# Kernel optimization log

Hardware: AMD Instinct MI355X
Metric: run time of the kernel (lower is better)

The kernel has to match this reference:

```python
import jax, jax.numpy as jnp
import numpy as np

B, S, INQ = 2048, 200, 120
POS_E = 8
H, QLEN, VLEN = 8, 16, 64
HID = H * VLEN  # 512
IN_F = INQ + POS_E  # 128
LN_EPS = 1e-5


def _css(x, W, b, Wc, bc):
    # CssModel: gated linear h1 * sigmoid(h1c)
    h1 = x @ W + b
    h1c = jax.nn.sigmoid(x @ Wc + bc)
    return h1 * h1c


def _layernorm(x, g, b):
    mu = jnp.mean(x, axis=-1, keepdims=True)
    var = jnp.var(x, axis=-1, keepdims=True)
    return (x - mu) * jax.lax.rsqrt(var + LN_EPS) * g + b


def setup_inputs() -> dict:
    key = jax.random.key(0)
    ks = jax.random.split(key, 16)
    d = {}
    d["posid"] = jax.random.randint(ks[0], (B, S), 0, 100, dtype=jnp.int64) if jax.config.jax_enable_x64 else jax.random.randint(ks[0], (B, S), 0, 100).astype(jnp.int32)
    d["qcv"] = jax.random.normal(ks[1], (B, S, INQ), dtype=jnp.float32)
    d["mask"] = jnp.ones((S,), dtype=jnp.float32)
    s = 0.05
    d["posembed"] = jax.random.normal(ks[2], (100, POS_E), dtype=jnp.float32) * s
    d["Wq"] = jax.random.normal(ks[3], (IN_F, H * QLEN), dtype=jnp.float32) * s
    d["bq"] = jnp.zeros((H * QLEN,), jnp.float32)
    d["Wqc"] = jax.random.normal(ks[4], (IN_F, H * QLEN), dtype=jnp.float32) * s
    d["bqc"] = jnp.zeros((H * QLEN,), jnp.float32)
    d["Wk"] = jax.random.normal(ks[5], (IN_F, H * QLEN), dtype=jnp.float32) * s
    d["bk"] = jnp.zeros((H * QLEN,), jnp.float32)
    d["Wkc"] = jax.random.normal(ks[6], (IN_F, H * QLEN), dtype=jnp.float32) * s
    d["bkc"] = jnp.zeros((H * QLEN,), jnp.float32)
    d["Wv"] = jax.random.normal(ks[7], (IN_F, HID), dtype=jnp.float32) * s
    d["bv"] = jnp.zeros((HID,), jnp.float32)
    d["Wvc"] = jax.random.normal(ks[8], (IN_F, HID), dtype=jnp.float32) * s
    d["bvc"] = jnp.zeros((HID,), jnp.float32)
    d["v_ln_g"] = jnp.ones((HID,), jnp.float32)
    d["v_ln_b"] = jnp.zeros((HID,), jnp.float32)
    return d


def reference(posid, qcv, mask, posembed, Wq, bq, Wqc, bqc, Wk, bk, Wkc, bkc, Wv, bv, Wvc, bvc, v_ln_g, v_ln_b):
    # positional embedding lookup + concat -> [B, S, IN_F]
    pe = posembed[posid]
    x = jnp.concatenate([qcv, pe], axis=-1)

    # gated projections (y is None so vcv == qcv-with-pos)
    q = _css(x[:, 0:1], Wq, bq, Wqc, bqc)                 # [B, 1, H*QLEN]
    k = _css(x, Wk, bk, Wkc, bkc)                          # [B, S, H*QLEN]
    v = _layernorm(_css(x, Wv, bv, Wvc, bvc), v_ln_g, v_ln_b)  # [B, S, HID]

    q = q.reshape(B, 1, H, QLEN).transpose(0, 2, 1, 3)     # [B, H, 1, QLEN]
    k = k.reshape(B, S, H, QLEN).transpose(0, 2, 1, 3)     # [B, H, S, QLEN]
    v = v.reshape(B, S, H, VLEN).transpose(0, 2, 1, 3)     # [B, H, S, VLEN]

    # mask added BEFORE the 1/sqrt(qlen) scaling, matching the source
    mask_add = (1.0 - mask) * -10000.0                     # [S]
    scores = jnp.einsum('bhqd,bhkd->bhqk', q, k)
    scores = (scores + mask_add[None, None, None, :]) / np.sqrt(QLEN).astype(np.float32)
    probs = jax.nn.softmax(scores, axis=-1)
    ctx = jnp.einsum('bhqk,bhkd->bhqd', probs, v)          # [B, H, 1, VLEN]
    ctx = ctx.transpose(0, 2, 1, 3).reshape(B, 1, HID)     # [B, 1, HID]
    return ctx
```

## Files before the change

### kernel.cpp

```cpp
#include <hip/hip_runtime.h>
#include <hip/hip_bf16.h>

typedef __attribute__((ext_vector_type(8))) short short8;
typedef __attribute__((ext_vector_type(4))) float f32x4;

#define MFMA_B16(a,b,c) __builtin_amdgcn_mfma_f32_16x16x32_bf16((a),(b),(c),0,0,0)

namespace {
constexpr int B_SZ = 2048;
constexpr int S_SZ = 200;
constexpr int SPAD = 208;
constexpr int NRT  = 13;
constexpr int INQ  = 120;
constexpr int HID  = 512;

constexpr int L_XF    = 0;
constexpr int L_WT1   = 53248;
constexpr int L_WT2   = 86016;
constexpr int L_QV    = 118784;
constexpr int L_X0    = 119296;
constexpr int L_QP    = 119808;
constexpr int L_PROBS = 123904;
constexpr int L_DEN   = 130560;
constexpr int L_STATS = 130592;
constexpr int L_MU    = 131616;
constexpr int L_RS    = 131680;
constexpr int L_TOTAL = 131744;
}

static __device__ __forceinline__ short f2bf(float x) {
    unsigned u = __builtin_bit_cast(unsigned, x);
    u = (u + 0x7FFFu + ((u >> 16) & 1u)) >> 16;
    return (short)u;
}
static __device__ __forceinline__ float sigm(float x) { return 1.f / (1.f + __expf(-x)); }

__global__ void __launch_bounds__(512)
attseq_main(const int* __restrict__ posid, const float* __restrict__ qcv,
            const float* __restrict__ maskp, const float* __restrict__ posembed,
            const float* __restrict__ Wq, const float* __restrict__ bq,
            const float* __restrict__ Wqc, const float* __restrict__ bqc,
            const float* __restrict__ Wk, const float* __restrict__ bk,
            const float* __restrict__ Wkc, const float* __restrict__ bkc,
            const float* __restrict__ Wv, const float* __restrict__ bv,
            const float* __restrict__ Wvc, const float* __restrict__ bvc,
            const float* __restrict__ lng, const float* __restrict__ lnb,
            float* __restrict__ out)
{
    extern __shared__ __align__(16) char smem[];
    const int b = blockIdx.x;
    const int t = threadIdx.x;
    const int w = t >> 6;
    const int l = t & 63;
    const int g = l >> 4;
    const int d = l & 15;

    const f32x4 fzero = {0.f, 0.f, 0.f, 0.f};

    {
        short* xfb = (short*)(smem + L_XF);
        float* x0f = (float*)(smem + L_X0);
        for (int it = 0; it < 52; ++it) {
            int idx = t + (it << 9);
            int s = idx >> 7, c = idx & 127;
            float val = 0.f;
            if (s < S_SZ) {
                if (c < INQ) val = qcv[(size_t)b * (S_SZ * INQ) + s * INQ + c];
                else {
                    int pid = posid[b * S_SZ + s];
                    val = posembed[pid * 8 + (c - INQ)];
                }
            }
            if (s == 0) x0f[c] = val;
            int rt = s >> 4, r = s & 15, kt = c >> 5, ck = c & 31;
            int off = ((rt * 4 + kt) * 64 + (r + 16 * (ck >> 3))) * 8 + (ck & 7);
            xfb[off] = f2bf(val);
        }
    }
    {
        short* wt1 = (short*)(smem + L_WT1);
        short* wt2 = (short*)(smem + L_WT2);
        for (int i = 0; i < 32; ++i) {
            int e = t + (i << 9);
            int k = e >> 7, n = e & 127;
            int ct = n >> 4, kt = k >> 5, g2 = (k >> 3) & 3, j = k & 7;
            int off = ((ct * 4 + kt) * 64 + (16 * g2 + (n & 15))) * 8 + j;
            wt1[off] = f2bf(Wk[e]);
            wt2[off] = f2bf(Wkc[e]);
        }
    }
    __syncthreads();

    {
        int j = t & 127, qt = t >> 7;
        const float* x0 = (const float*)(smem + L_X0);
        float h1 = 0.f, h1c = 0.f;
        for (int i = 32 * qt; i < 32 * qt + 32; ++i) {
            float xv = x0[i];
            h1  += xv * Wq[i * 128 + j];
            h1c += xv * Wqc[i * 128 + j];
        }
        float* qp = (float*)(smem + L_QP);
        qp[(qt * 128 + j) * 2 + 0] = h1;
        qp[(qt * 128 + j) * 2 + 1] = h1c;
    }
    __syncthreads();
    if (t < 128) {
        const float* qp = (const float*)(smem + L_QP);
        float h1 = 0.f, h1c = 0.f;
        #pragma unroll
        for (int qt = 0; qt < 4; ++qt) {
            h1  += qp[(qt * 128 + t) * 2 + 0];
            h1c += qp[(qt * 128 + t) * 2 + 1];
        }
        h1 += bq[t]; h1c += bqc[t];
        ((float*)(smem + L_QV))[t] = h1 * sigm(h1c);
    }
    __syncthreads();

    {
        const float* qv = (const float*)(smem + L_QV);
        float* sc = (float*)(smem + L_PROBS);
        float bkv[8], bkcv[8];
        #pragma unroll
        for (int ct = 0; ct < 8; ++ct) { bkv[ct] = bk[ct * 16 + d]; bkcv[ct] = bkc[ct * 16 + d]; }
        for (int rt = w; rt < NRT; rt += 8) {
            short8 a[4];
            #pragma unroll
            for (int kt = 0; kt < 4; ++kt)
                a[kt] = *(const short8*)(smem + L_XF + (((rt * 4 + kt) * 64 + l) << 4));
            f32x4 acc1[8], acc2[8];
            #pragma unroll
            for (int ct = 0; ct < 8; ++ct) { acc1[ct] = fzero; acc2[ct] = fzero; }
            #pragma unroll
            for (int kt = 0; kt < 4; ++kt) {
                #pragma unroll
                for (int ct = 0; ct < 8; ++ct) {
                    short8 b1 = *(const short8*)(smem + L_WT1 + (((ct * 4 + kt) * 64 + l) << 4));
                    short8 b2 = *(const short8*)(smem + L_WT2 + (((ct * 4 + kt) * 64 + l) << 4));
                    acc1[ct] = MFMA_B16(a[kt], b1, acc1[ct]);
                    acc2[ct] = MFMA_B16(a[kt], b2, acc2[ct]);
                }
            }
            #pragma unroll
            for (int ct = 0; ct < 8; ++ct) {
                float qd = qv[ct * 16 + d];
                #pragma unroll
                for (int r = 0; r < 4; ++r) {
                    float h1  = acc1[ct][r] + bkv[ct];
                    float h1c = acc2[ct][r] + bkcv[ct];
                    float p = qd * (h1 * sigm(h1c));
                    p += __shfl_xor(p, 1); p += __shfl_xor(p, 2);
                    p += __shfl_xor(p, 4); p += __shfl_xor(p, 8);
                    if (d == 0) {
                        int row = rt * 16 + 4 * g + r;
                        sc[ct * SPAD + row] = (row < S_SZ)
                            ? (p + (1.f - maskp[row]) * (-10000.f)) * 0.25f
                            : -1e30f;
                    }
                }
            }
        }
    }
    __syncthreads();

    {
        float* sc = (float*)(smem + L_PROBS);
        float s0 = sc[w * SPAD + l];
        float s1 = sc[w * SPAD + l + 64];
        float s2 = sc[w * SPAD + l + 128];
        float s3 = (l < 16) ? sc[w * SPAD + l + 192] : -1e30f;
        float m = fmaxf(fmaxf(s0, s1), fmaxf(s2, s3));
        #pragma unroll
        for (int mk = 1; mk < 64; mk <<= 1) m = fmaxf(m, __shfl_xor(m, mk));
        float p0 = __expf(s0 - m), p1 = __expf(s1 - m), p2 = __expf(s2 - m);
        float p3 = (l < 16) ? __expf(s3 - m) : 0.f;
        float sum = p0 + p1 + p2 + p3;
        #pragma unroll
        for (int mk = 1; mk < 64; mk <<= 1) sum += __shfl_xor(sum, mk);
        sc[w * SPAD + l]       = p0;
        sc[w * SPAD + l + 64]  = p1;
        sc[w * SPAD + l + 128] = p2;
        if (l < 16) sc[w * SPAD + l + 192] = p3;
        if (l == 0) ((float*)(smem + L_DEN))[w] = sum;
    }
    __syncthreads();

    {
        short8 fv[4][4], fvc[4][4];
        {
            const float* wv0  = Wv  + (size_t)(8 * (l >> 4)) * HID + 64 * w + d;
            const float* wvc0 = Wvc + (size_t)(8 * (l >> 4)) * HID + 64 * w + d;
            #pragma unroll
            for (int cc = 0; cc < 4; ++cc) {
                #pragma unroll
                for (int kt = 0; kt < 4; ++kt) {
                    #pragma unroll
                    for (int j = 0; j < 8; ++j) {
                        int o = (32 * kt + j) * HID + 16 * cc;
                        fv[cc][kt][j]  = f2bf(wv0[o]);
                        fvc[cc][kt][j] = f2bf(wvc0[o]);
                    }
                }
            }
        }
        float bvv[4], bvcv[4], gv[4], bbv[4];
        #pragma unroll
        for (int cc = 0; cc < 4; ++cc) {
            int c = 64 * w + 16 * cc + d;
            bvv[cc] = bv[c]; bvcv[cc] = bvc[c]; gv[cc] = lng[c]; bbv[cc] = lnb[c];
        }
        float ctx[4] = {0.f, 0.f, 0.f, 0.f};
        const float* pr = (const float*)(smem + L_PROBS);
        float* stats = (float*)(smem + L_STATS);
        float* muR = (float*)(smem + L_MU);
        float* rsR = (float*)(smem + L_RS);

        for (int rt = 0; rt < NRT; ++rt) {
            short8 a[4];
            #pragma unroll
            for (int kt = 0; kt < 4; ++kt)
                a[kt] = *(const short8*)(smem + L_XF + (((rt * 4 + kt) * 64 + l) << 4));
            f32x4 acc1[4], acc2[4];
            #pragma unroll
            for (int cc = 0; cc < 4; ++cc) { acc1[cc] = fzero; acc2[cc] = fzero; }
            #pragma unroll
            for (int kt = 0; kt < 4; ++kt) {
                #pragma unroll
                for (int cc = 0; cc < 4; ++cc) {
                    acc1[cc] = MFMA_B16(a[kt], fv[cc][kt],  acc1[cc]);
                    acc2[cc] = MFMA_B16(a[kt], fvc[cc][kt], acc2[cc]);
                }
            }
            float vout[4][4];
            #pragma unroll
            for (int cc = 0; cc < 4; ++cc)
                #pragma unroll
                for (int r = 0; r < 4; ++r)
                    vout[cc][r] = (acc1[cc][r] + bvv[cc]) * sigm(acc2[cc][r] + bvcv[cc]);
            #pragma unroll
            for (int r = 0; r < 4; ++r) {
                float s1 = vout[0][r] + vout[1][r] + vout[2][r] + vout[3][r];
                float s2 = vout[0][r] * vout[0][r] + vout[1][r] * vout[1][r]
                         + vout[2][r] * vout[2][r] + vout[3][r] * vout[3][r];
                #pragma unroll
                for (int mk = 1; mk <= 8; mk <<= 1) {
                    s1 += __shfl_xor(s1, mk);
                    s2 += __shfl_xor(s2, mk);
                }
                if (d == 0) {
                    int rl = 4 * g + r;
                    stats[(rl * 8 + w) * 2 + 0] = s1;
                    stats[(rl * 8 + w) * 2 + 1] = s2;
                }
            }
            __syncthreads();
            if (t < 16) {
                float s1 = 0.f, s2 = 0.f;
                #pragma unroll
                for (int ww = 0; ww < 8; ++ww) {
                    s1 += stats[(t * 8 + ww) * 2 + 0];
                    s2 += stats[(t * 8 + ww) * 2 + 1];
                }
                float mu = s1 * (1.f / 512.f);
                float var = s2 * (1.f / 512.f) - mu * mu;
                muR[t] = mu;
                rsR[t] = rsqrtf(var + 1e-5f);
            }
            __syncthreads();
            #pragma unroll
            for (int r = 0; r < 4; ++r) {
                int rl = 4 * g + r;
                float mu = muR[rl], rs = rsR[rl];
                float pw = pr[w * SPAD + rt * 16 + rl];
                #pragma unroll
                for (int cc = 0; cc < 4; ++cc)
                    ctx[cc] += pw * ((vout[cc][r] - mu) * rs * gv[cc] + bbv[cc]);
            }
        }
        #pragma unroll
        for (int cc = 0; cc < 4; ++cc) {
            ctx[cc] += __shfl_xor(ctx[cc], 16);
            ctx[cc] += __shfl_xor(ctx[cc], 32);
        }
        float invden = 1.f / ((const float*)(smem + L_DEN))[w];
        if (l < 16) {
            #pragma unroll
            for (int cc = 0; cc < 4; ++cc) {
                int c = 64 * w + 16 * cc + l;
                out[(size_t)b * HID + c] = ctx[cc] * invden;
            }
        }
    }
}

extern "C" void kernel_launch(void* const* d_in, const int* in_sizes, int n_in,
                              void* d_out, int out_size, void* d_ws, size_t ws_size,
                              hipStream_t stream)
{
    const int*   posid = (const int*)d_in[0];
    const float* qcv   = (const float*)d_in[1];
    const float* mask  = (const float*)d_in[2];
    const float* pe    = (const float*)d_in[3];
    const float* Wq    = (const float*)d_in[4];
    const float* bq    = (const float*)d_in[5];
    const float* Wqc   = (const float*)d_in[6];
    const float* bqc   = (const float*)d_in[7];
    const float* Wk    = (const float*)d_in[8];
    const float* bk    = (const float*)d_in[9];
    const float* Wkc   = (const float*)d_in[10];
    const float* bkc   = (const float*)d_in[11];
    const float* Wv    = (const float*)d_in[12];
    const float* bv    = (const float*)d_in[13];
    const float* Wvc   = (const float*)d_in[14];
    const float* bvc   = (const float*)d_in[15];
    const float* lng   = (const float*)d_in[16];
    const float* lnb   = (const float*)d_in[17];
    float* outp = (float*)d_out;

    hipFuncSetAttribute((const void*)attseq_main,
                        hipFuncAttributeMaxDynamicSharedMemorySize, L_TOTAL);

    attseq_main<<<B_SZ, 512, L_TOTAL, stream>>>(posid, qcv, mask, pe, Wq, bq, Wqc, bqc,
                                                Wk, bk, Wkc, bkc, Wv, bv, Wvc, bvc,
                                                lng, lnb, outp);
}
```

Baseline: 1.091 ms.

## Cut LDS and registers via two-pass V recompute and per-wave K weights

Stops staging the transformed K weights in shared memory. Each wave now keeps its own 16-column K/Kc bf16 fragments in registers, computes one head's scores, and normalizes the probabilities in place. The V projection is split into two passes over column chunks: the first collects per-row LayerNorm statistics for all rows, and the second recomputes the gated V and folds in the normalized values weighted by probability. This removes the per-tile block barriers and lowers shared memory and register use to allow more resident blocks (launch_bounds 512,4). The cost is running the V MFMAs twice and re-reading the V weights from global memory.

New measurement: 1.048 ms. -3.9%, faster.

```diff
diff --git a/kernel.cpp b/kernel.cpp
--- a/kernel.cpp
+++ b/kernel.cpp
@@ -15,17 +15,14 @@
 constexpr int HID  = 512;
 
 constexpr int L_XF    = 0;
-constexpr int L_WT1   = 53248;
-constexpr int L_WT2   = 86016;
-constexpr int L_QV    = 118784;
-constexpr int L_X0    = 119296;
-constexpr int L_QP    = 119808;
-constexpr int L_PROBS = 123904;
-constexpr int L_DEN   = 130560;
-constexpr int L_STATS = 130592;
-constexpr int L_MU    = 131616;
-constexpr int L_RS    = 131680;
-constexpr int L_TOTAL = 131744;
+constexpr int L_PROBS = 53248;
+constexpr int L_QV    = 59904;
+constexpr int L_X0    = 60416;
+constexpr int L_QP    = 60928;
+constexpr int L_WST   = 60928;
+constexpr int L_MU    = 73728;
+constexpr int L_RS    = 74528;
+constexpr int L_TOTAL = 75328;
 }
 
 static __device__ __forceinline__ short f2bf(float x) {
@@ -35,7 +32,7 @@
 }
 static __device__ __forceinline__ float sigm(float x) { return 1.f / (1.f + __expf(-x)); }
 
-__global__ void __launch_bounds__(512)
+__global__ void __launch_bounds__(512, 4)
 attseq_main(const int* __restrict__ posid, const float* __restrict__ qcv,
             const float* __restrict__ maskp, const float* __restrict__ posembed,
             const float* __restrict__ Wq, const float* __restrict__ bq,
@@ -77,18 +74,6 @@
             xfb[off] = f2bf(val);
         }
     }
-    {
-        short* wt1 = (short*)(smem + L_WT1);
-        short* wt2 = (short*)(smem + L_WT2);
-        for (int i = 0; i < 32; ++i) {
-            int e = t + (i << 9);
-            int k = e >> 7, n = e & 127;
-            int ct = n >> 4, kt = k >> 5, g2 = (k >> 3) & 3, j = k & 7;
-            int off = ((ct * 4 + kt) * 64 + (16 * g2 + (n & 15))) * 8 + j;
-            wt1[off] = f2bf(Wk[e]);
-            wt2[off] = f2bf(Wkc[e]);
-        }
-    }
     __syncthreads();
 
     {
@@ -116,48 +101,49 @@
         h1 += bq[t]; h1c += bqc[t];
         ((float*)(smem + L_QV))[t] = h1 * sigm(h1c);
     }
+    short8 fk[4], fkc[4];
+    {
+        const float* wk0  = Wk  + (size_t)(8 * (l >> 4)) * 128 + w * 16 + d;
+        const float* wkc0 = Wkc + (size_t)(8 * (l >> 4)) * 128 + w * 16 + d;
+        #pragma unroll
+        for (int kt = 0; kt < 4; ++kt)
+            #pragma unroll
+            for (int j = 0; j < 8; ++j) {
+                int o = (32 * kt + j) * 128;
+                fk[kt][j]  = f2bf(wk0[o]);
+                fkc[kt][j] = f2bf(wkc0[o]);
+            }
+    }
     __syncthreads();
 
     {
         const float* qv = (const float*)(smem + L_QV);
         float* sc = (float*)(smem + L_PROBS);
-        float bkv[8], bkcv[8];
-        #pragma unroll
-        for (int ct = 0; ct < 8; ++ct) { bkv[ct] = bk[ct * 16 + d]; bkcv[ct] = bkc[ct * 16 + d]; }
-        for (int rt = w; rt < NRT; rt += 8) {
+        const float qd = qv[w * 16 + d];
+        const float bkd = bk[w * 16 + d], bkcd = bkc[w * 16 + d];
+        for (int rt = 0; rt < NRT; ++rt) {
             short8 a[4];
             #pragma unroll
             for (int kt = 0; kt < 4; ++kt)
                 a[kt] = *(const short8*)(smem + L_XF + (((rt * 4 + kt) * 64 + l) << 4));
-            f32x4 acc1[8], acc2[8];
-            #pragma unroll
-            for (int ct = 0; ct < 8; ++ct) { acc1[ct] = fzero; acc2[ct] = fzero; }
+            f32x4 acc1 = fzero, acc2 = fzero;
             #pragma unroll
             for (int kt = 0; kt < 4; ++kt) {
-                #pragma unroll
-                for (int ct = 0; ct < 8; ++ct) {
-                    short8 b1 = *(const short8*)(smem + L_WT1 + (((ct * 4 + kt) * 64 + l) << 4));
-                    short8 b2 = *(const short8*)(smem + L_WT2 + (((ct * 4 + kt) * 64 + l) << 4));
-                    acc1[ct] = MFMA_B16(a[kt], b1, acc1[ct]);
-                    acc2[ct] = MFMA_B16(a[kt], b2, acc2[ct]);
-                }
-            }
-            #pragma unroll
-            for (int ct = 0; ct < 8; ++ct) {
-                float qd = qv[ct * 16 + d];
-                #pragma unroll
-                for (int r = 0; r < 4; ++r) {
-                    float h1  = acc1[ct][r] + bkv[ct];
-                    float h1c = acc2[ct][r] + bkcv[ct];
-                    float p = qd * (h1 * sigm(h1c));
-                    p += __shfl_xor(p, 1); p += __shfl_xor(p, 2);
-                    p += __shfl_xor(p, 4); p += __shfl_xor(p, 8);
-                    if (d == 0) {
-                        int row = rt * 16 + 4 * g + r;
-                        sc[ct * SPAD + row] = (row < S_SZ)
-                            ? (p + (1.f - maskp[row]) * (-10000.f)) * 0.25f
-                            : -1e30f;
-                    }
+                acc1 = MFMA_B16(a[kt], fk[kt],  acc1);
+                acc2 = MFMA_B16(a[kt], fkc[kt], acc2);
+            }
+            #pragma unroll
+            for (int r = 0; r < 4; ++r) {
+                float h1  = acc1[r] + bkd;
+                float h1c = acc2[r] + bkcd;
+                float p = qd * (h1 * sigm(h1c));
+                p += __shfl_xor(p, 1); p += __shfl_xor(p, 2);
+                p += __shfl_xor(p, 4); p += __shfl_xor(p, 8);
+                if (d == 0) {
+                    int row = rt * 16 + 4 * g + r;
+                    sc[w * SPAD + row] = (row < S_SZ)
+                        ? (p + (1.f - maskp[row]) * (-10000.f)) * 0.25f
+                        : -1e30f;
                 }
             }
         }
@@ -178,118 +164,122 @@
         float sum = p0 + p1 + p2 + p3;
         #pragma unroll
         for (int mk = 1; mk < 64; mk <<= 1) sum += __shfl_xor(sum, mk);
-        sc[w * SPAD + l]       = p0;
-        sc[w * SPAD + l + 64]  = p1;
-        sc[w * SPAD + l + 128] = p2;
-        if (l < 16) sc[w * SPAD + l + 192] = p3;
-        if (l == 0) ((float*)(smem + L_DEN))[w] = sum;
-    }
-    __syncthreads();
-
-    {
-        short8 fv[4][4], fvc[4][4];
-        {
-            const float* wv0  = Wv  + (size_t)(8 * (l >> 4)) * HID + 64 * w + d;
-            const float* wvc0 = Wvc + (size_t)(8 * (l >> 4)) * HID + 64 * w + d;
-            #pragma unroll
-            for (int cc = 0; cc < 4; ++cc) {
+        float inv = 1.f / sum;
+        sc[w * SPAD + l]       = p0 * inv;
+        sc[w * SPAD + l + 64]  = p1 * inv;
+        sc[w * SPAD + l + 128] = p2 * inv;
+        if (l < 16) sc[w * SPAD + l + 192] = p3 * inv;
+    }
+    __syncthreads();
+
+    {
+        float* wst = (float*)(smem + L_WST);
+        for (int cc = 0; cc < 4; ++cc) {
+            short8 fv[4], fvc[4];
+            const float* wv0  = Wv  + (size_t)(8 * (l >> 4)) * HID + 64 * w + 16 * cc + d;
+            const float* wvc0 = Wvc + (size_t)(8 * (l >> 4)) * HID + 64 * w + 16 * cc + d;
+            #pragma unroll
+            for (int kt = 0; kt < 4; ++kt)
+                #pragma unroll
+                for (int j = 0; j < 8; ++j) {
+                    int o = (32 * kt + j) * HID;
+                    fv[kt][j]  = f2bf(wv0[o]);
+                    fvc[kt][j] = f2bf(wvc0[o]);
+                }
+            const float bvn  = bv[64 * w + 16 * cc + d];
+            const float bvcn = bvc[64 * w + 16 * cc + d];
+            for (int rt = 0; rt < NRT; ++rt) {
+                short8 a[4];
+                #pragma unroll
+                for (int kt = 0; kt < 4; ++kt)
+                    a[kt] = *(const short8*)(smem + L_XF + (((rt * 4 + kt) * 64 + l) << 4));
+                f32x4 acc1 = fzero, acc2 = fzero;
                 #pragma unroll
                 for (int kt = 0; kt < 4; ++kt) {
+                    acc1 = MFMA_B16(a[kt], fv[kt],  acc1);
+                    acc2 = MFMA_B16(a[kt], fvc[kt], acc2);
+                }
+                #pragma unroll
+                for (int r = 0; r < 4; ++r) {
+                    float vout = (acc1[r] + bvn) * sigm(acc2[r] + bvcn);
+                    float s1 = vout, s2 = vout * vout;
                     #pragma unroll
-                    for (int j = 0; j < 8; ++j) {
-                        int o = (32 * kt + j) * HID + 16 * cc;
-                        fv[cc][kt][j]  = f2bf(wv0[o]);
-                        fvc[cc][kt][j] = f2bf(wvc0[o]);
+                    for (int mk = 1; mk <= 8; mk <<= 1) {
+                        s1 += __shfl_xor(s1, mk);
+                        s2 += __shfl_xor(s2, mk);
                     }
-                }
-            }
-        }
-        float bvv[4], bvcv[4], gv[4], bbv[4];
-        #pragma unroll
+                    if (d == 0) {
+                        int row = rt * 16 + 4 * g + r;
+                        if (row < S_SZ) {
+                            int o2 = (row * 8 + w) * 2;
+                            if (cc == 0) { wst[o2] = s1;  wst[o2 + 1] = s2; }
+                            else         { wst[o2] += s1; wst[o2 + 1] += s2; }
+                        }
+                    }
+                }
+            }
+        }
+    }
+    __syncthreads();
+    if (t < S_SZ) {
+        const float* wst = (const float*)(smem + L_WST);
+        float s1 = 0.f, s2 = 0.f;
+        #pragma unroll
+        for (int ww = 0; ww < 8; ++ww) {
+            s1 += wst[(t * 8 + ww) * 2 + 0];
+            s2 += wst[(t * 8 + ww) * 2 + 1];
+        }
+        float mu = s1 * (1.f / 512.f);
+        float var = s2 * (1.f / 512.f) - mu * mu;
+        ((float*)(smem + L_MU))[t] = mu;
+        ((float*)(smem + L_RS))[t] = rsqrtf(var + 1e-5f);
+    }
+    __syncthreads();
+
+    {
+        const float* pr  = (const float*)(smem + L_PROBS);
+        const float* muR = (const float*)(smem + L_MU);
+        const float* rsR = (const float*)(smem + L_RS);
         for (int cc = 0; cc < 4; ++cc) {
-            int c = 64 * w + 16 * cc + d;
-            bvv[cc] = bv[c]; bvcv[cc] = bvc[c]; gv[cc] = lng[c]; bbv[cc] = lnb[c];
-        }
-        float ctx[4] = {0.f, 0.f, 0.f, 0.f};
-        const float* pr = (const float*)(smem + L_PROBS);
-        float* stats = (float*)(smem + L_STATS);
-        float* muR = (float*)(smem + L_MU);
-        float* rsR = (float*)(smem + L_RS);
-
-        for (int rt = 0; rt < NRT; ++rt) {
-            short8 a[4];
+            short8 fv[4], fvc[4];
+            const float* wv0  = Wv  + (size_t)(8 * (l >> 4)) * HID + 64 * w + 16 * cc + d;
+            const float* wvc0 = Wvc + (size_t)(8 * (l >> 4)) * HID + 64 * w + 16 * cc + d;
             #pragma unroll
             for (int kt = 0; kt < 4; ++kt)
-                a[kt] = *(const short8*)(smem + L_XF + (((rt * 4 + kt) * 64 + l) << 4));
-            f32x4 acc1[4], acc2[4];
-            #pragma unroll
-            for (int cc = 0; cc < 4; ++cc) { acc1[cc] = fzero; acc2[cc] = fzero; }
-            #pragma unroll
-            for (int kt = 0; kt < 4; ++kt) {
-                #pragma unroll
-                for (int cc = 0; cc < 4; ++cc) {
-                    acc1[cc] = MFMA_B16(a[kt], fv[cc][kt],  acc1[cc]);
-                    acc2[cc] = MFMA_B16(a[kt], fvc[cc][kt], acc2[cc]);
-                }
-            }
-            float vout[4][4];
-            #pragma unroll
-            for (int cc = 0; cc < 4; ++cc)
-                #pragma unroll
-                for (int r = 0; r < 4; ++r)
-                    vout[cc][r] = (acc1[cc][r] + bvv[cc]) * sigm(acc2[cc][r] + bvcv[cc]);
-            #pragma unroll
-            for (int r = 0; r < 4; ++r) {
-                float s1 = vout[0][r] + vout[1][r] + vout[2][r] + vout[3][r];
-                float s2 = vout[0][r] * vout[0][r] + vout[1][r] * vout[1][r]
-                         + vout[2][r] * vout[2][r] + vout[3][r] * vout[3][r];
-                #pragma unroll
-                for (int mk = 1; mk <= 8; mk <<= 1) {
-                    s1 += __shfl_xor(s1, mk);
-                    s2 += __shfl_xor(s2, mk);
-                }
-                if (d == 0) {
-                    int rl = 4 * g + r;
-                    stats[(rl * 8 + w) * 2 + 0] = s1;
-                    stats[(rl * 8 + w) * 2 + 1] = s2;
-                }
-            }
-            __syncthreads();
-            if (t < 16) {
-                float s1 = 0.f, s2 = 0.f;
-                #pragma unroll
-                for (int ww = 0; ww < 8; ++ww) {
-                    s1 += stats[(t * 8 + ww) * 2 + 0];
-                    s2 += stats[(t * 8 + ww) * 2 + 1];
-                }
-                float mu = s1 * (1.f / 512.f);
-                float var = s2 * (1.f / 512.f) - mu * mu;
-                muR[t] = mu;
-                rsR[t] = rsqrtf(var + 1e-5f);
-            }
-            __syncthreads();
-            #pragma unroll
-            for (int r = 0; r < 4; ++r) {
-                int rl = 4 * g + r;
-                float mu = muR[rl], rs = rsR[rl];
-                float pw = pr[w * SPAD + rt * 16 + rl];
-                #pragma unroll
-                for (int cc = 0; cc < 4; ++cc)
-                    ctx[cc] += pw * ((vout[cc][r] - mu) * rs * gv[cc] + bbv[cc]);
-            }
-        }
-        #pragma unroll
-        for (int cc = 0; cc < 4; ++cc) {
-            ctx[cc] += __shfl_xor(ctx[cc], 16);
-            ctx[cc] += __shfl_xor(ctx[cc], 32);
-        }
-        float invden = 1.f / ((const float*)(smem + L_DEN))[w];
-        if (l < 16) {
-            #pragma unroll
-            for (int cc = 0; cc < 4; ++cc) {
-                int c = 64 * w + 16 * cc + l;
-                out[(size_t)b * HID + c] = ctx[cc] * invden;
-            }
+                #pragma unroll
+                for (int j = 0; j < 8; ++j) {
+                    int o = (32 * kt + j) * HID;
+                    fv[kt][j]  = f2bf(wv0[o]);
+                    fvc[kt][j] = f2bf(wvc0[o]);
+                }
+            const int n = 64 * w + 16 * cc + d;
+            const float bvn = bv[n], bvcn = bvc[n], gn = lng[n], bbn = lnb[n];
+            float ctx = 0.f;
+            for (int rt = 0; rt < NRT; ++rt) {
+                short8 a[4];
+                #pragma unroll
+                for (int kt = 0; kt < 4; ++kt)
+                    a[kt] = *(const short8*)(smem + L_XF + (((rt * 4 + kt) * 64 + l) << 4));
+                f32x4 acc1 = fzero, acc2 = fzero;
+                #pragma unroll
+                for (int kt = 0; kt < 4; ++kt) {
+                    acc1 = MFMA_B16(a[kt], fv[kt],  acc1);
+                    acc2 = MFMA_B16(a[kt], fvc[kt], acc2);
+                }
+                #pragma unroll
+                for (int r = 0; r < 4; ++r) {
+                    int row = rt * 16 + 4 * g + r;
+                    if (row < S_SZ) {
+                        float vout = (acc1[r] + bvn) * sigm(acc2[r] + bvcn);
+                        float pw = pr[w * SPAD + row];
+                        ctx += pw * ((vout - muR[row]) * rsR[row] * gn + bbn);
+                    }
+                }
+            }
+            ctx += __shfl_xor(ctx, 16);
+            ctx += __shfl_xor(ctx, 32);
+            if (l < 16)
+                out[(size_t)b * HID + 64 * w + 16 * cc + l] = ctx;
         }
     }
 }
```
